# Kernel optimization log

Hardware: AMD Instinct MI355X
Metric: run time of the kernel (lower is better)

## Reference

```python
import jax, jax.numpy as jnp
import numpy as np

N_PATCH = 676
K_SEL = int(676 * 0.8)  # 540
HEADS = 16
LN_EPS = 1e-5


def _layernorm(t, w, b):
    mu = t.mean(-1, keepdims=True)
    var = ((t - mu) ** 2).mean(-1, keepdims=True)
    return (t - mu) * jax.lax.rsqrt(var + LN_EPS) * w + b


def _attention(t, w_qkv, b_qkv, w_out, b_out):
    # t: [S, B, C] (seq-first, like torch nn.MultiheadAttention)
    S, B, C = t.shape
    D = C // HEADS
    qkv = t @ w_qkv.T + b_qkv                       # [S, B, 3C]
    q, k, v = jnp.split(qkv, 3, axis=-1)
    def heads(a):
        return a.reshape(S, B, HEADS, D).transpose(1, 2, 0, 3)  # [B,H,S,D]
    q, k, v = heads(q), heads(k), heads(v)
    scores = jnp.einsum('bhqd,bhkd->bhqk', q, k) / jnp.sqrt(jnp.asarray(D, t.dtype))
    attn = jax.nn.softmax(scores, axis=-1)
    o = jnp.einsum('bhqk,bhkd->bhqd', attn, v)      # [B,H,S,D]
    o = o.transpose(2, 0, 1, 3).reshape(S, B, C)
    return o @ w_out.T + b_out


def _mlp(t, w_fc1, b_fc1, w_fc2, b_fc2):
    h = t @ w_fc1.T + b_fc1
    h = h * jax.nn.sigmoid(1.702 * h)  # CLIP QuickGELU
    return h @ w_fc2.T + b_fc2


def setup_inputs() -> dict:
    key = jax.random.key(0)
    ks = jax.random.split(key, 6)
    C, B, L = 1024, 32, 77
    inp = {
        'x': jax.random.normal(ks[0], (1 + N_PATCH, B, C), jnp.float32),
        'lang_tokens': jax.random.normal(ks[1], (L, B, C), jnp.float32),
        'ln1_w': jnp.ones((C,), jnp.float32),
        'ln1_b': jnp.zeros((C,), jnp.float32),
        'ln2_w': jnp.ones((C,), jnp.float32),
        'ln2_b': jnp.zeros((C,), jnp.float32),
        'w_qkv': jax.random.normal(ks[2], (3 * C, C), jnp.float32) * 0.02,
        'b_qkv': jnp.zeros((3 * C,), jnp.float32),
        'w_out': jax.random.normal(ks[3], (C, C), jnp.float32) * 0.02,
        'b_out': jnp.zeros((C,), jnp.float32),
        'w_fc1': jax.random.normal(ks[4], (4 * C, C), jnp.float32) * 0.02,
        'b_fc1': jnp.zeros((4 * C,), jnp.float32),
        'w_fc2': jax.random.normal(ks[5], (C, 4 * C), jnp.float32) * 0.02,
        'b_fc2': jnp.zeros((C,), jnp.float32),
    }
    return inp


def reference(x, lang_tokens, ln1_w, ln1_b, ln2_w, ln2_b, w_qkv, b_qkv,
              w_out, b_out, w_fc1, b_fc1, w_fc2, b_fc2):
    Nfull, B, C = x.shape
    cls_x = x[:1]            # [1, B, C]
    xt = x[1:]               # [676, B, C]

    # per-token language-alignment score: [676, B]
    score = jnp.einsum('nbc,lbc->nbl', xt, lang_tokens).mean(-1)

    # top-k selection per batch column; torch boolean-mask gather preserves
    # the ORIGINAL token order within the high/low sets -> sort the indices.
    order = jnp.argsort(-score, axis=0)                 # descending
    high_idx = jnp.sort(order[:K_SEL], axis=0)          # [540, B]
    low_idx = jnp.sort(order[K_SEL:], axis=0)           # [136, B]

    delta_x = jnp.take_along_axis(xt, high_idx[:, :, None], axis=0)  # [540,B,C]
    low_x = jnp.take_along_axis(xt, low_idx[:, :, None], axis=0)     # [136,B,C]
    low_score = jnp.take_along_axis(score, low_idx, axis=0)[:, :, None]
    low_tok = (low_x * jax.nn.softmax(low_score, axis=0)).sum(0, keepdims=True)

    seq = jnp.concatenate([cls_x, delta_x, low_tok], axis=0)  # [542, B, C]
    d = _attention(_layernorm(seq, ln1_w, ln1_b), w_qkv, b_qkv, w_out, b_out)

    barange = jnp.arange(B)[None, :]
    temple = jnp.zeros_like(xt)
    temple = temple.at[high_idx, barange].set(d[1:-1])
    temple = temple.at[low_idx, barange].set(
        jnp.broadcast_to(d[-1:], (N_PATCH - K_SEL, B, C)))

    xt = xt + temple
    cls_x = cls_x + d[:1]
    x = jnp.concatenate([cls_x, xt], axis=0)
    x = x + _mlp(_layernorm(x, ln2_w, ln2_b), w_fc1, b_fc1, w_fc2, b_fc2)
    return x
```

## Files before the change

kernel.cpp:

```cpp
#include <hip/hip_runtime.h>
#include <hip/hip_bf16.h>

typedef unsigned short u16;
typedef __attribute__((ext_vector_type(4))) float f32x4;
typedef __attribute__((ext_vector_type(8))) short s16x8;

#define DEVI __device__ __forceinline__

static constexpr int NPATCH = 676;
static constexpr int KSEL   = 540;
static constexpr int NLOW   = 136;
static constexpr int BB     = 32;
static constexpr int CC     = 1024;
static constexpr int S      = 542;
static constexpr int SP     = 576;
static constexpr int M1P    = SP * BB;
static constexpr int NTOK   = 677;
static constexpr int M2     = NTOK * BB;
static constexpr int M2P    = 21760;
static constexpr int NKT    = SP / 64;
static constexpr int NQC    = 5;

DEVI u16 f2bf(float f) {
  unsigned u = __float_as_uint(f);
  u += 0x7fffu + ((u >> 16) & 1u);
  return (u16)(u >> 16);
}
DEVI float bf2f(u16 h) { return __uint_as_float(((unsigned)h) << 16); }
DEVI float ex2(float x) { float r; asm("v_exp_f32 %0, %1" : "=v"(r) : "v"(x)); return r; }

DEVI void gld16(const void* g, void* l) {
  __builtin_amdgcn_global_load_lds((const __attribute__((address_space(1))) void*)g,
                                   (__attribute__((address_space(3))) void*)l,
                                   16, 0, 0);
}

DEVI void BAR() {
  asm volatile("" ::: "memory");
  __builtin_amdgcn_s_barrier();
  asm volatile("" ::: "memory");
}
#define LGKM0() do { asm volatile("s_waitcnt lgkmcnt(0)" ::: "memory"); \
                     __builtin_amdgcn_sched_barrier(0); } while (0)
#define VMC(N) asm volatile("s_waitcnt vmcnt(" #N ")" ::: "memory")


__global__ void k_f2bf4(const float* __restrict__ in, u16* __restrict__ out, int n4) {
  int i = blockIdx.x * blockDim.x + threadIdx.x;
  if (i >= n4) return;
  float4 v = ((const float4*)in)[i];
  unsigned long long p = (unsigned long long)f2bf(v.x)
                       | ((unsigned long long)f2bf(v.y) << 16)
                       | ((unsigned long long)f2bf(v.z) << 32)
                       | ((unsigned long long)f2bf(v.w) << 48);
  *(unsigned long long*)&out[(long)i * 4] = p;
}

__global__ void k_langmean(const float* __restrict__ lang, float* __restrict__ lm) {
  int b = blockIdx.x, t = threadIdx.x;
  float a0 = 0, a1 = 0, a2 = 0, a3 = 0;
  for (int l = 0; l < 77; l++) {
    float4 v = ((const float4*)(lang + ((long)l * BB + b) * CC))[t];
    a0 += v.x; a1 += v.y; a2 += v.z; a3 += v.w;
  }
  const float inv = 1.f / 77.f;
  float4 o; o.x = a0 * inv; o.y = a1 * inv; o.z = a2 * inv; o.w = a3 * inv;
  ((float4*)(lm + b * CC))[t] = o;
}

__global__ void k_score(const float* __restrict__ x, const float* __restrict__ lm,
                        float* __restrict__ score) {
  int nb = blockIdx.x;
  int n = nb >> 5, b = nb & 31;
  int t = threadIdx.x;
  float4 xv = ((const float4*)(x + ((long)(n + 1) * BB + b) * CC))[t];
  float4 lv = ((const float4*)(lm + b * CC))[t];
  float s = xv.x * lv.x + xv.y * lv.y + xv.z * lv.z + xv.w * lv.w;
  for (int m = 1; m < 64; m <<= 1) s += __shfl_xor(s, m);
  __shared__ float sm[4];
  if ((t & 63) == 0) sm[t >> 6] = s;
  __syncthreads();
  if (t == 0) score[n * BB + b] = sm[0] + sm[1] + sm[2] + sm[3];
}

__global__ void k_select(const float* __restrict__ score, float* __restrict__ wall,
                         int* __restrict__ rowmap, int* __restrict__ selsrc,
                         int* __restrict__ lowlist) {
  int b = blockIdx.x, t = threadIdx.x;
  __shared__ float sc[NPATCH];
  __shared__ int hf[NPATCH];
  __shared__ float red[2];
  if (t < NPATCH) sc[t] = score[t * BB + b];
  __syncthreads();
  int high = 0;
  if (t < NPATCH) {
    float s = sc[t];
    int r = 0;
    for (int m = 0; m < NPATCH; m++) {
      float sm_ = sc[m];
      r += (sm_ > s) || (sm_ == s && m < t);
    }
    high = (r < KSEL);
    hf[t] = high;
  }
  __syncthreads();
  if (t < NPATCH) {
    int p = 0;
    for (int m = 0; m < t; m++) p += hf[m];
    if (high) {
      rowmap[b * NPATCH + t] = 1 + p;
      selsrc[b * S + 1 + p] = t + 1;
    } else {
      rowmap[b * NPATCH + t] = S - 1;
      lowlist[b * NLOW + (t - p)] = t;
    }
  }
  if (t == 0) selsrc[b * S + 0] = 0;
  __syncthreads();
  if (t == 0) {
    float m = -3e38f;
    for (int i = 0; i < NPATCH; i++) if (!hf[i]) m = fmaxf(m, sc[i]);
    float d = 0;
    for (int i = 0; i < NPATCH; i++) if (!hf[i]) d += __expf(sc[i] - m);
    red[0] = m; red[1] = d;
  }
  __syncthreads();
  if (t < NPATCH) wall[b * NPATCH + t] = hf[t] ? 0.f : __expf(sc[t] - red[0]) / red[1];
}

__global__ void k_lowtok(const float* __restrict__ x, const float* __restrict__ wall,
                         const int* __restrict__ lowlist, float* __restrict__ lowtok) {
  int b = blockIdx.x, ch = blockIdx.y;
  int c = ch * 256 + threadIdx.x;
  float acc = 0.f;
  for (int i = 0; i < NLOW; i++) {
    int n = lowlist[b * NLOW + i];
    acc += wall[b * NPATCH + n] * x[((long)(n + 1) * BB + b) * CC + c];
  }
  lowtok[b * CC + c] = acc;
}

__global__ void k_lnseq(const float* __restrict__ x, const float* __restrict__ lowtok,
                        const int* __restrict__ selsrc, const float* __restrict__ w,
                        const float* __restrict__ bias, u16* __restrict__ out) {
  int s = blockIdx.x, b = blockIdx.y, t = threadIdx.x;
  u16* orow = out + ((long)b * SP + s) * CC;
  if (s >= S) { *(unsigned long long*)&orow[4 * t] = 0ULL; return; }
  const float* src;
  if (s == 0)          src = x + (long)b * CC;
  else if (s == S - 1) src = lowtok + (long)b * CC;
  else                 src = x + ((long)selsrc[b * S + s] * BB + b) * CC;
  float4 v = ((const float4*)src)[t];
  float ss = v.x + v.y + v.z + v.w;
  float s2 = v.x * v.x + v.y * v.y + v.z * v.z + v.w * v.w;
  for (int k = 1; k < 64; k <<= 1) { ss += __shfl_xor(ss, k); s2 += __shfl_xor(s2, k); }
  __shared__ float sa[4], sb[4];
  if ((t & 63) == 0) { sa[t >> 6] = ss; sb[t >> 6] = s2; }
  __syncthreads();
  ss = sa[0] + sa[1] + sa[2] + sa[3];
  s2 = sb[0] + sb[1] + sb[2] + sb[3];
  float mu = ss * (1.f / CC);
  float var = s2 * (1.f / CC) - mu * mu;
  float rs = rsqrtf(var + 1e-5f);
  int c = 4 * t;
  unsigned long long p = (unsigned long long)f2bf((v.x - mu) * rs * w[c]     + bias[c])
                       | ((unsigned long long)f2bf((v.y - mu) * rs * w[c + 1] + bias[c + 1]) << 16)
                       | ((unsigned long long)f2bf((v.z - mu) * rs * w[c + 2] + bias[c + 2]) << 32)
                       | ((unsigned long long)f2bf((v.w - mu) * rs * w[c + 3] + bias[c + 3]) << 48);
  *(unsigned long long*)&orow[4 * t] = p;
}

__global__ void k_scatln(const float* __restrict__ x, const u16* __restrict__ dbuf,
                         const int* __restrict__ rowmap, const float* __restrict__ w,
                         const float* __restrict__ bias, float* __restrict__ out,
                         u16* __restrict__ lnout) {
  int m = blockIdx.x, t = threadIdx.x;
  u16* orow = lnout + (long)m * CC;
  if (m >= M2) { *(unsigned long long*)&orow[4 * t] = 0ULL; return; }
  int nf = m >> 5, b = m & 31;
  int srow = (nf == 0) ? 0 : rowmap[b * NPATCH + (nf - 1)];
  float4 xv = ((const float4*)(x + (long)m * CC))[t];
  unsigned long long dp = *(const unsigned long long*)&dbuf[((long)b * SP + srow) * CC + 4 * t];
  float4 v;
  v.x = xv.x + bf2f((u16)(dp));
  v.y = xv.y + bf2f((u16)(dp >> 16));
  v.z = xv.z + bf2f((u16)(dp >> 32));
  v.w = xv.w + bf2f((u16)(dp >> 48));
  ((float4*)(out + (long)m * CC))[t] = v;
  float ss = v.x + v.y + v.z + v.w;
  float s2 = v.x * v.x + v.y * v.y + v.z * v.z + v.w * v.w;
  for (int k = 1; k < 64; k <<= 1) { ss += __shfl_xor(ss, k); s2 += __shfl_xor(s2, k); }
  __shared__ float sa[4], sb[4];
  if ((t & 63) == 0) { sa[t >> 6] = ss; sb[t >> 6] = s2; }
  __syncthreads();
  ss = sa[0] + sa[1] + sa[2] + sa[3];
  s2 = sb[0] + sb[1] + sb[2] + sb[3];
  float mu = ss * (1.f / CC);
  float var = s2 * (1.f / CC) - mu * mu;
  float rs = rsqrtf(var + 1e-5f);
  int c = 4 * t;
  unsigned long long p = (unsigned long long)f2bf((v.x - mu) * rs * w[c]     + bias[c])
                       | ((unsigned long long)f2bf((v.y - mu) * rs * w[c + 1] + bias[c + 1]) << 16)
                       | ((unsigned long long)f2bf((v.z - mu) * rs * w[c + 2] + bias[c + 2]) << 32)
                       | ((unsigned long long)f2bf((v.w - mu) * rs * w[c + 3] + bias[c + 3]) << 48);
  *(unsigned long long*)&orow[4 * t] = p;
}


struct Epi {
  const float* bias;
  u16* obf;
  float* of;
  u16 *qb, *kb, *vtb;
  int mvalid, ldc;
};

DEVI void stage_half(u16* dst, const u16* src, int ld) {
  int t = threadIdx.x;
  int c = t & 7;
  int r0 = t >> 3;
  gld16(src + (long)r0 * ld + ((c ^ (r0 & 7)) << 3), dst + (t << 3));
  int r1 = r0 + 64;
  gld16(src + (long)r1 * ld + ((c ^ (r1 & 7)) << 3), dst + 4096 + (t << 3));
}

DEVI s16x8 frag(const u16* half, int rh, int kk, int h4) {
  int chunk = ((kk << 2) | h4) ^ (rh & 7);
  return *(const s16x8*)(half + rh * 64 + chunk * 8);
}

template<int MODE>
__global__ __launch_bounds__(512, 2) void k_gemm8(const u16* __restrict__ A, int lda,
                                                  const u16* __restrict__ Bw, int ldb,
                                                  int K, Epi e) {
  __shared__ __align__(16) u16 lds[2][2][2][8192];
  int t = threadIdx.x;
  int lane = t & 63, w = t >> 6;
  int h4 = lane >> 4, r = lane & 15;
  int wr = w >> 2, wc = w & 3;
  int MBk = gridDim.x, NBk = gridDim.y;
  int nwg = MBk * NBk;
  int orig = blockIdx.y * MBk + blockIdx.x;
  int q8 = nwg >> 3, r8 = nwg & 7, xcd = orig & 7, rk = orig >> 3;
  int wgid = (xcd < r8 ? xcd * (q8 + 1) : r8 * (q8 + 1) + (xcd - r8) * q8) + rk;
  int bm = wgid / NBk, bn = wgid % NBk;

  const u16* Asrc = A + (long)bm * 256 * lda;
  const u16* Bsrc = Bw + (long)bn * 256 * ldb;
  int NT = K >> 6;

  f32x4 acc[8][4];
#pragma unroll
  for (int i = 0; i < 8; i++)
#pragma unroll
    for (int j = 0; j < 4; j++) acc[i][j] = {0.f, 0.f, 0.f, 0.f};

  stage_half(lds[0][0][0], Asrc, lda);
  stage_half(lds[0][0][1], Asrc + (long)128 * lda, lda);
  stage_half(lds[0][1][0], Bsrc, ldb);
  stage_half(lds[0][1][1], Bsrc + (long)128 * ldb, ldb);
  {
    const u16* B1 = Bsrc + (NT > 1 ? 64 : 0);
    stage_half(lds[1][1][0], B1, ldb);
    stage_half(lds[1][1][1], B1 + (long)128 * ldb, ldb);
  }
  VMC(4);
  BAR();

  for (int kt = 0; kt < NT; kt++) {
    int buf = kt & 1;
    const u16* Ah = lds[buf][0][wr];
    const u16* Bh = lds[buf][1][wc >> 1];
    int rbB = (wc & 1) << 6;
    int ka = (kt + 1 < NT) ? kt + 1 : NT - 1;
    int kb = (kt + 2 < NT) ? kt + 2 : NT - 1;
    const u16* Aps = Asrc + ka * 64;
    const u16* Bps = Bsrc + kb * 64;
    u16* AdL = lds[(kt + 1) & 1][0][0];
    u16* AdH = lds[(kt + 1) & 1][0][1];
    u16* BdL = lds[buf][1][0];
    u16* BdH = lds[buf][1][1];

    s16x8 a8[8], b8[8];
#pragma unroll
    for (int i = 0; i < 4; i++) {
      a8[i * 2]     = frag(Ah, i * 16 + r, 0, h4);
      a8[i * 2 + 1] = frag(Ah, i * 16 + r, 1, h4);
    }
#pragma unroll
    for (int j = 0; j < 2; j++) {
      b8[j * 2]     = frag(Bh, rbB + j * 16 + r, 0, h4);
      b8[j * 2 + 1] = frag(Bh, rbB + j * 16 + r, 1, h4);
    }
    stage_half(AdL, Aps, lda);
    BAR(); LGKM0();
    __builtin_amdgcn_s_setprio(1);
#pragma unroll
    for (int i = 0; i < 4; i++)
#pragma unroll
      for (int j = 0; j < 2; j++) {
        acc[i][j] = __builtin_amdgcn_mfma_f32_16x16x32_bf16(a8[i * 2],     b8[j * 2],     acc[i][j], 0, 0, 0);
        acc[i][j] = __builtin_amdgcn_mfma_f32_16x16x32_bf16(a8[i * 2 + 1], b8[j * 2 + 1], acc[i][j], 0, 0, 0);
      }
    __builtin_amdgcn_s_setprio(0);
    BAR();
#pragma unroll
    for (int j = 0; j < 2; j++) {
      b8[4 + j * 2]     = frag(Bh, rbB + (j + 2) * 16 + r, 0, h4);
      b8[4 + j * 2 + 1] = frag(Bh, rbB + (j + 2) * 16 + r, 1, h4);
    }
    stage_half(AdH, Aps + (long)128 * lda, lda);
    BAR(); LGKM0();
    __builtin_amdgcn_s_setprio(1);
#pragma unroll
    for (int i = 0; i < 4; i++)
#pragma unroll
      for (int j = 0; j < 2; j++) {
        acc[i][j + 2] = __builtin_amdgcn_mfma_f32_16x16x32_bf16(a8[i * 2],     b8[4 + j * 2],     acc[i][j + 2], 0, 0, 0);
        acc[i][j + 2] = __builtin_amdgcn_mfma_f32_16x16x32_bf16(a8[i * 2 + 1], b8[4 + j * 2 + 1], acc[i][j + 2], 0, 0, 0);
      }
    __builtin_amdgcn_s_setprio(0);
    BAR();
#pragma unroll
    for (int i = 0; i < 4; i++) {
      a8[i * 2]     = frag(Ah, (i + 4) * 16 + r, 0, h4);
      a8[i * 2 + 1] = frag(Ah, (i + 4) * 16 + r, 1, h4);
    }
    stage_half(BdL, Bps, ldb);
    BAR(); LGKM0();
    __builtin_amdgcn_s_setprio(1);
#pragma unroll
    for (int i = 0; i < 4; i++)
#pragma unroll
      for (int j = 0; j < 2; j++) {
        acc[i + 4][j] = __builtin_amdgcn_mfma_f32_16x16x32_bf16(a8[i * 2],     b8[j * 2],     acc[i + 4][j], 0, 0, 0);
        acc[i + 4][j] = __builtin_amdgcn_mfma_f32_16x16x32_bf16(a8[i * 2 + 1], b8[j * 2 + 1], acc[i + 4][j], 0, 0, 0);
      }
    __builtin_amdgcn_s_setprio(0);
    BAR();
    stage_half(BdH, Bps + (long)128 * ldb, ldb);
    BAR();
    __builtin_amdgcn_s_setprio(1);
#pragma unroll
    for (int i = 0; i < 4; i++)
#pragma unroll
      for (int j = 0; j < 2; j++) {
        acc[i + 4][j + 2] = __builtin_amdgcn_mfma_f32_16x16x32_bf16(a8[i * 2],     b8[4 + j * 2],     acc[i + 4][j + 2], 0, 0, 0);
        acc[i + 4][j + 2] = __builtin_amdgcn_mfma_f32_16x16x32_bf16(a8[i * 2 + 1], b8[4 + j * 2 + 1], acc[i + 4][j + 2], 0, 0, 0);
      }
    __builtin_amdgcn_s_setprio(0);
    VMC(4);
    BAR();
  }

  const float QSC = 0.125f * 1.44269504088896f;
#pragma unroll
  for (int i = 0; i < 8; i++) {
    int m0 = bm * 256 + wr * 128 + i * 16 + 4 * h4;
#pragma unroll
    for (int j = 0; j < 4; j++) {
      int n = bn * 256 + wc * 64 + j * 16 + r;
      float bias = (MODE == 3 && e.bias == nullptr) ? 0.f : e.bias[n];
      if (MODE == 0) {
        int part = n >> 10, cc = n & 1023;
        int hh = cc >> 6, dd = cc & 63;
        int b0 = m0 / SP, s0 = m0 % SP;
        if (part == 2) {
          u16 pk[4];
#pragma unroll
          for (int tt = 0; tt < 4; tt++) pk[tt] = f2bf(acc[i][j][tt] + bias);
          *(unsigned long long*)&e.vtb[((long)(b0 * 16 + hh) * 64 + dd) * SP + s0] =
              *(unsigned long long*)pk;
        } else {
          u16* dst = (part == 0 ? e.qb : e.kb) + ((long)(b0 * 16 + hh) * SP + s0) * 64 + dd;
          float scl = (part == 0) ? QSC : 1.f;
#pragma unroll
          for (int tt = 0; tt < 4; tt++) dst[tt * 64] = f2bf((acc[i][j][tt] + bias) * scl);
        }
      } else if (MODE == 1) {
#pragma unroll
        for (int tt = 0; tt < 4; tt++)
          e.obf[(long)(m0 + tt) * e.ldc + n] = f2bf(acc[i][j][tt] + bias);
      } else if (MODE == 2) {
#pragma unroll
        for (int tt = 0; tt < 4; tt++) {
          float v = acc[i][j][tt] + bias;
          v = v / (1.f + __expf(-1.702f * v));
          e.obf[(long)(m0 + tt) * e.ldc + n] = f2bf(v);
        }
      } else {
#pragma unroll
        for (int tt = 0; tt < 4; tt++) {
          int m = m0 + tt;
          if (m < e.mvalid) e.of[(long)m * CC + n] += acc[i][j][tt] + bias;
        }
      }
    }
  }
}


DEVI void stage64(u16* dst, const u16* src, int ld) {
  int t = threadIdx.x;
  int c = t & 7, r0 = t >> 3;
  gld16(src + (long)r0 * ld + ((c ^ (r0 & 7)) << 3), dst + t * 8);
  int r1 = r0 + 32;
  gld16(src + (long)r1 * ld + ((c ^ (r1 & 7)) << 3), dst + 2048 + t * 8);
}

__global__ __launch_bounds__(256, 4) void k_attn2(const u16* __restrict__ qb,
                                                  const u16* __restrict__ kb,
                                                  const u16* __restrict__ vtb,
                                                  u16* __restrict__ aout) {
  __shared__ __align__(16) u16 Kt[2][4096];
  __shared__ __align__(16) u16 Vt[2][4096];
  __shared__ __align__(16) u16 Pl[4][1024];

  int nwg = gridDim.x;
  int orig = blockIdx.x;
  int q8 = nwg >> 3, r8 = nwg & 7, xcd = orig & 7, rk = orig >> 3;
  int wgid = (xcd < r8 ? xcd * (q8 + 1) : r8 * (q8 + 1) + (xcd - r8) * q8) + rk;
  int bh = wgid / NQC, qc = wgid % NQC;
  int b = bh >> 4, hh = bh & 15;
  int t = threadIdx.x, w = t >> 6, lane = t & 63;
  int h4 = lane >> 4, r = lane & 15;

  const u16* Q  = qb  + (long)bh * SP * 64;
  const u16* Kg = kb  + (long)bh * SP * 64;
  const u16* Vg = vtb + (long)bh * 64 * SP;

  int qt[2];
  bool act[2];
  s16x8 aq0[2], aq1[2];
  f32x4 o[2][4];
  float mM[2][4], lL[2][4];
#pragma unroll
  for (int sub = 0; sub < 2; sub++) {
    qt[sub] = qc * 8 + w * 2 + sub;
    act[sub] = qt[sub] < SP / 16;
    if (act[sub]) {
      aq0[sub] = *(const s16x8*)&Q[(qt[sub] * 16 + r) * 64 + h4 * 8];
      aq1[sub] = *(const s16x8*)&Q[(qt[sub] * 16 + r) * 64 + 32 + h4 * 8];
    }
#pragma unroll
    for (int i = 0; i < 4; i++) { o[sub][i] = {0.f, 0.f, 0.f, 0.f}; mM[sub][i] = -1e30f; lL[sub][i] = 0.f; }
  }

  stage64(Kt[0], Kg, 64);
  stage64(Vt[0], Vg, SP);
  VMC(0);
  BAR();

  for (int kt = 0; kt < NKT; kt++) {
    int cur = kt & 1;
    if (kt + 1 < NKT) {
      stage64(Kt[cur ^ 1], Kg + (kt + 1) * 64 * 64, 64);
      stage64(Vt[cur ^ 1], Vg + (kt + 1) * 64, SP);
    }
    int kv0 = kt * 64;
    const u16* Kc = Kt[cur];
    const u16* Vc = Vt[cur];
#pragma unroll
    for (int sub = 0; sub < 2; sub++) {
      if (!act[sub]) continue;
      f32x4 sf[4];
#pragma unroll
      for (int f = 0; f < 4; f++) {
        sf[f] = {0.f, 0.f, 0.f, 0.f};
        sf[f] = __builtin_amdgcn_mfma_f32_16x16x32_bf16(aq0[sub], frag(Kc, f * 16 + r, 0, h4), sf[f], 0, 0, 0);
        sf[f] = __builtin_amdgcn_mfma_f32_16x16x32_bf16(aq1[sub], frag(Kc, f * 16 + r, 1, h4), sf[f], 0, 0, 0);
      }
      if (kv0 + 64 > S) {
#pragma unroll
        for (int f = 0; f < 4; f++)
          if (kv0 + f * 16 + r >= S) {
#pragma unroll
            for (int tt = 0; tt < 4; tt++) sf[f][tt] = -1e30f;
          }
      }
      float mx[4];
#pragma unroll
      for (int tt = 0; tt < 4; tt++)
        mx[tt] = fmaxf(fmaxf(sf[0][tt], sf[1][tt]), fmaxf(sf[2][tt], sf[3][tt]));
      for (int msk = 1; msk < 16; msk <<= 1) {
#pragma unroll
        for (int tt = 0; tt < 4; tt++) mx[tt] = fmaxf(mx[tt], __shfl_xor(mx[tt], msk));
      }
      int need = 0;
#pragma unroll
      for (int tt = 0; tt < 4; tt++) need |= (mx[tt] > mM[sub][tt] + 8.f);
      if (__any(need)) {
#pragma unroll
        for (int tt = 0; tt < 4; tt++) {
          float mn = fmaxf(mM[sub][tt], mx[tt]);
          float sc = ex2(mM[sub][tt] - mn);
          mM[sub][tt] = mn;
          lL[sub][tt] *= sc;
#pragma unroll
          for (int nf = 0; nf < 4; nf++) o[sub][nf][tt] *= sc;
        }
      }
      float rs[4];
#pragma unroll
      for (int tt = 0; tt < 4; tt++) {
        float m_ = mM[sub][tt];
        float p0 = ex2(sf[0][tt] - m_), p1 = ex2(sf[1][tt] - m_);
        float p2 = ex2(sf[2][tt] - m_), p3 = ex2(sf[3][tt] - m_);
        sf[0][tt] = p0; sf[1][tt] = p1; sf[2][tt] = p2; sf[3][tt] = p3;
        rs[tt] = (p0 + p1) + (p2 + p3);
      }
      for (int msk = 1; msk < 16; msk <<= 1) {
#pragma unroll
        for (int tt = 0; tt < 4; tt++) rs[tt] += __shfl_xor(rs[tt], msk);
      }
#pragma unroll
      for (int tt = 0; tt < 4; tt++) lL[sub][tt] += rs[tt];
      u16* Pw = Pl[w];
#pragma unroll
      for (int f = 0; f < 4; f++)
#pragma unroll
        for (int tt = 0; tt < 4; tt++) {
          int q = 4 * h4 + tt;
          int chunk = (f * 2 + (r >> 3)) ^ (q & 7);
          Pw[q * 64 + chunk * 8 + (r & 7)] = f2bf(sf[f][tt]);
        }
      s16x8 pa0 = frag(Pw, r, 0, h4);
      s16x8 pa1 = frag(Pw, r, 1, h4);
#pragma unroll
      for (int nf = 0; nf < 4; nf++) {
        o[sub][nf] = __builtin_amdgcn_mfma_f32_16x16x32_bf16(pa0, frag(Vc, nf * 16 + r, 0, h4), o[sub][nf], 0, 0, 0);
        o[sub][nf] = __builtin_amdgcn_mfma_f32_16x16x32_bf16(pa1, frag(Vc, nf * 16 + r, 1, h4), o[sub][nf], 0, 0, 0);
      }
    }
    VMC(0);
    BAR();
  }

#pragma unroll
  for (int sub = 0; sub < 2; sub++) {
    if (!act[sub]) continue;
    float inv[4];
#pragma unroll
    for (int tt = 0; tt < 4; tt++) inv[tt] = 1.f / lL[sub][tt];
#pragma unroll
    for (int nf = 0; nf < 4; nf++)
#pragma unroll
      for (int tt = 0; tt < 4; tt++) {
        int q = qt[sub] * 16 + 4 * h4 + tt;
        if (q < S) aout[((long)b * SP + q) * CC + hh * 64 + nf * 16 + r] = f2bf(o[sub][nf][tt] * inv[tt]);
      }
  }
}


extern "C" void kernel_launch(void* const* d_in, const int* in_sizes, int n_in,
                              void* d_out, int out_size, void* d_ws, size_t ws_size,
                              hipStream_t stream) {
  const float* x    = (const float*)d_in[0];
  const float* lang = (const float*)d_in[1];
  const float* ln1w = (const float*)d_in[2];
  const float* ln1b = (const float*)d_in[3];
  const float* ln2w = (const float*)d_in[4];
  const float* ln2b = (const float*)d_in[5];
  const float* wqkv = (const float*)d_in[6];
  const float* bqkv = (const float*)d_in[7];
  const float* wout = (const float*)d_in[8];
  const float* bout = (const float*)d_in[9];
  const float* wfc1 = (const float*)d_in[10];
  const float* bfc1 = (const float*)d_in[11];
  const float* wfc2 = (const float*)d_in[12];
  const float* bfc2 = (const float*)d_in[13];
  float* out = (float*)d_out;
  char* ws = (char*)d_ws;
  const size_t MiB = 1ull << 20;

  float* lm      = (float*)(ws + 0 * MiB);
  float* score   = (float*)(ws + 1 * MiB);
  float* wall    = (float*)(ws + 2 * MiB);
  int*   rowmap  = (int*)  (ws + 3 * MiB);
  int*   selsrc  = (int*)  (ws + 4 * MiB);
  int*   lowlist = (int*)  (ws + 5 * MiB);
  float* lowtok  = (float*)(ws + 6 * MiB);
  u16* wqb  = (u16*)(ws + 7 * MiB);
  u16* wob  = (u16*)(ws + 13 * MiB);
  u16* wf1b = (u16*)(ws + 15 * MiB);
  u16* wf2b = (u16*)(ws + 23 * MiB);
  u16* qbuf = (u16*)(ws + 31 * MiB);
  u16* kbuf = (u16*)(ws + 67 * MiB);
  u16* vtb  = (u16*)(ws + 103 * MiB);
  u16* regA = (u16*)(ws + 139 * MiB);
  u16* lnseq = regA;
  u16* aout  = regA;
  u16* dbuf  = vtb;
  u16* ln2bf = qbuf;
  u16* hbuf  = (u16*)(ws + 74 * MiB);

  {
    int n4;
    n4 = 3072 * 1024 / 4; k_f2bf4<<<(n4 + 255) / 256, 256, 0, stream>>>(wqkv, wqb, n4);
    n4 = 1024 * 1024 / 4; k_f2bf4<<<(n4 + 255) / 256, 256, 0, stream>>>(wout, wob, n4);
    n4 = 4096 * 1024 / 4; k_f2bf4<<<(n4 + 255) / 256, 256, 0, stream>>>(wfc1, wf1b, n4);
    n4 = 1024 * 4096 / 4; k_f2bf4<<<(n4 + 255) / 256, 256, 0, stream>>>(wfc2, wf2b, n4);
  }

  k_langmean<<<BB, 256, 0, stream>>>(lang, lm);
  k_score<<<NPATCH * BB, 256, 0, stream>>>(x, lm, score);
  k_select<<<BB, 1024, 0, stream>>>(score, wall, rowmap, selsrc, lowlist);
  k_lowtok<<<dim3(BB, 4), 256, 0, stream>>>(x, wall, lowlist, lowtok);
  k_lnseq<<<dim3(SP, BB), 256, 0, stream>>>(x, lowtok, selsrc, ln1w, ln1b, lnseq);

  {
    Epi e = {};
    e.bias = bqkv; e.qb = qbuf; e.kb = kbuf; e.vtb = vtb; e.mvalid = M1P;
    k_gemm8<0><<<dim3(M1P / 256, 3072 / 256), 512, 0, stream>>>(lnseq, 1024, wqb, 1024, 1024, e);
  }

  k_attn2<<<BB * 16 * NQC, 256, 0, stream>>>(qbuf, kbuf, vtb, aout);

  {
    Epi e = {};
    e.bias = bout; e.obf = dbuf; e.mvalid = M1P; e.ldc = 1024;
    k_gemm8<1><<<dim3(M1P / 256, 1024 / 256), 512, 0, stream>>>(aout, 1024, wob, 1024, 1024, e);
  }

  k_scatln<<<M2P, 256, 0, stream>>>(x, dbuf, rowmap, ln2w, ln2b, out, ln2bf);

  for (int c = 0; c < 2; c++) {
    Epi e2 = {};
    e2.bias = bfc1 + c * 2048; e2.obf = hbuf; e2.mvalid = M2P; e2.ldc = 2048;
    k_gemm8<2><<<dim3(M2P / 256, 2048 / 256), 512, 0, stream>>>(ln2bf, 1024, wf1b + (long)c * 2048 * 1024, 1024, 1024, e2);
    Epi e3 = {};
    e3.bias = (c == 0 ? bfc2 : nullptr); e3.of = out; e3.mvalid = M2;
    k_gemm8<3><<<dim3(M2P / 256, 1024 / 256), 512, 0, stream>>>(hbuf, 2048, wf2b + c * 2048, 4096, 2048, e3);
  }
}
```

Before: 1.177 ms.

## Replace 256x256 pipelined GEMM with simpler 128x128 double-buffered kernel

Swaps the hand-scheduled 256x256 tile, 8-wave GEMM, with its interleaved staging, priority hints and fine-grained barriers, for a 128x128 tile, 4-wave kernel. The new kernel uses K-steps of 32 with plain double buffering and a new swizzled LDS layout. All four projection/MLP GEMMs launch with four times as many blocks and higher occupancy. The cost is lower data reuse per tile, more global and LDS traffic per FLOP, and dropping the carefully overlapped schedule.

```diff
diff --git a/kernel.cpp b/kernel.cpp
--- a/kernel.cpp
+++ b/kernel.cpp
@@ -40,8 +40,6 @@
   __builtin_amdgcn_s_barrier();
   asm volatile("" ::: "memory");
 }
-#define LGKM0() do { asm volatile("s_waitcnt lgkmcnt(0)" ::: "memory"); \
-                     __builtin_amdgcn_sched_barrier(0); } while (0)
 #define VMC(N) asm volatile("s_waitcnt vmcnt(" #N ")" ::: "memory")
 
 
@@ -215,13 +213,30 @@
   int mvalid, ldc;
 };
 
-DEVI void stage_half(u16* dst, const u16* src, int ld) {
+DEVI void stage32(u16* dst, const u16* src, int ld) {
   int t = threadIdx.x;
-  int c = t & 7;
-  int r0 = t >> 3;
-  gld16(src + (long)r0 * ld + ((c ^ (r0 & 7)) << 3), dst + (t << 3));
-  int r1 = r0 + 64;
-  gld16(src + (long)r1 * ld + ((c ^ (r1 & 7)) << 3), dst + 4096 + (t << 3));
+#pragma unroll
+  for (int q = 0; q < 2; q++) {
+    int s = t + q * 256;
+    int R = s >> 3, clp = s & 7;
+    int lc = clp ^ (R & 7);
+    int m = 2 * R + (lc >> 2), kc = lc & 3;
+    gld16(src + (long)m * ld + kc * 8, dst + s * 8);
+  }
+}
+
+DEVI s16x8 frag32(const u16* tile, int m, int h4) {
+  int R = m >> 1;
+  int phys = ((((m & 1) << 2) | h4) ^ (R & 7));
+  return *(const s16x8*)(tile + R * 64 + phys * 8);
+}
+
+DEVI void stage64(u16* dst, const u16* src, int ld) {
+  int t = threadIdx.x;
+  int c = t & 7, r0 = t >> 3;
+  gld16(src + (long)r0 * ld + ((c ^ (r0 & 7)) << 3), dst + t * 8);
+  int r1 = r0 + 32;
+  gld16(src + (long)r1 * ld + ((c ^ (r1 & 7)) << 3), dst + 2048 + t * 8);
 }
 
 DEVI s16x8 frag(const u16* half, int rh, int kk, int h4) {
@@ -230,14 +245,14 @@
 }
 
 template<int MODE>
-__global__ __launch_bounds__(512, 2) void k_gemm8(const u16* __restrict__ A, int lda,
+__global__ __launch_bounds__(256, 4) void k_gemm3(const u16* __restrict__ A, int lda,
                                                   const u16* __restrict__ Bw, int ldb,
                                                   int K, Epi e) {
-  __shared__ __align__(16) u16 lds[2][2][2][8192];
+  __shared__ __align__(16) u16 lds[2][2][4096];
   int t = threadIdx.x;
   int lane = t & 63, w = t >> 6;
   int h4 = lane >> 4, r = lane & 15;
-  int wr = w >> 2, wc = w & 3;
+  int wr = w >> 1, wc = w & 1;
   int MBk = gridDim.x, NBk = gridDim.y;
   int nwg = MBk * NBk;
   int orig = blockIdx.y * MBk + blockIdx.x;
@@ -245,121 +260,48 @@
   int wgid = (xcd < r8 ? xcd * (q8 + 1) : r8 * (q8 + 1) + (xcd - r8) * q8) + rk;
   int bm = wgid / NBk, bn = wgid % NBk;
 
-  const u16* Asrc = A + (long)bm * 256 * lda;
-  const u16* Bsrc = Bw + (long)bn * 256 * ldb;
-  int NT = K >> 6;
-
-  f32x4 acc[8][4];
-#pragma unroll
-  for (int i = 0; i < 8; i++)
+  const u16* Asrc = A + (long)bm * 128 * lda;
+  const u16* Bsrc = Bw + (long)bn * 128 * ldb;
+  int NT = K >> 5;
+
+  f32x4 acc[4][4];
+#pragma unroll
+  for (int i = 0; i < 4; i++)
 #pragma unroll
     for (int j = 0; j < 4; j++) acc[i][j] = {0.f, 0.f, 0.f, 0.f};
 
-  stage_half(lds[0][0][0], Asrc, lda);
-  stage_half(lds[0][0][1], Asrc + (long)128 * lda, lda);
-  stage_half(lds[0][1][0], Bsrc, ldb);
-  stage_half(lds[0][1][1], Bsrc + (long)128 * ldb, ldb);
-  {
-    const u16* B1 = Bsrc + (NT > 1 ? 64 : 0);
-    stage_half(lds[1][1][0], B1, ldb);
-    stage_half(lds[1][1][1], B1 + (long)128 * ldb, ldb);
-  }
-  VMC(4);
-  BAR();
+  stage32(lds[0][0], Asrc, lda);
+  stage32(lds[0][1], Bsrc, ldb);
+  __syncthreads();
 
   for (int kt = 0; kt < NT; kt++) {
-    int buf = kt & 1;
-    const u16* Ah = lds[buf][0][wr];
-    const u16* Bh = lds[buf][1][wc >> 1];
-    int rbB = (wc & 1) << 6;
-    int ka = (kt + 1 < NT) ? kt + 1 : NT - 1;
-    int kb = (kt + 2 < NT) ? kt + 2 : NT - 1;
-    const u16* Aps = Asrc + ka * 64;
-    const u16* Bps = Bsrc + kb * 64;
-    u16* AdL = lds[(kt + 1) & 1][0][0];
-    u16* AdH = lds[(kt + 1) & 1][0][1];
-    u16* BdL = lds[buf][1][0];
-    u16* BdH = lds[buf][1][1];
-
-    s16x8 a8[8], b8[8];
-#pragma unroll
-    for (int i = 0; i < 4; i++) {
-      a8[i * 2]     = frag(Ah, i * 16 + r, 0, h4);
-      a8[i * 2 + 1] = frag(Ah, i * 16 + r, 1, h4);
-    }
-#pragma unroll
-    for (int j = 0; j < 2; j++) {
-      b8[j * 2]     = frag(Bh, rbB + j * 16 + r, 0, h4);
-      b8[j * 2 + 1] = frag(Bh, rbB + j * 16 + r, 1, h4);
-    }
-    stage_half(AdL, Aps, lda);
-    BAR(); LGKM0();
-    __builtin_amdgcn_s_setprio(1);
+    int cur = kt & 1;
+    if (kt + 1 < NT) {
+      stage32(lds[cur ^ 1][0], Asrc + (kt + 1) * 32, lda);
+      stage32(lds[cur ^ 1][1], Bsrc + (kt + 1) * 32, ldb);
+    }
+    const u16* At = lds[cur][0];
+    const u16* Bt = lds[cur][1];
+    s16x8 af[4], bf[4];
+#pragma unroll
+    for (int i = 0; i < 4; i++) af[i] = frag32(At, wr * 64 + i * 16 + r, h4);
+#pragma unroll
+    for (int j = 0; j < 4; j++) bf[j] = frag32(Bt, wc * 64 + j * 16 + r, h4);
 #pragma unroll
     for (int i = 0; i < 4; i++)
 #pragma unroll
-      for (int j = 0; j < 2; j++) {
-        acc[i][j] = __builtin_amdgcn_mfma_f32_16x16x32_bf16(a8[i * 2],     b8[j * 2],     acc[i][j], 0, 0, 0);
-        acc[i][j] = __builtin_amdgcn_mfma_f32_16x16x32_bf16(a8[i * 2 + 1], b8[j * 2 + 1], acc[i][j], 0, 0, 0);
-      }
-    __builtin_amdgcn_s_setprio(0);
-    BAR();
-#pragma unroll
-    for (int j = 0; j < 2; j++) {
-      b8[4 + j * 2]     = frag(Bh, rbB + (j + 2) * 16 + r, 0, h4);
-      b8[4 + j * 2 + 1] = frag(Bh, rbB + (j + 2) * 16 + r, 1, h4);
-    }
-    stage_half(AdH, Aps + (long)128 * lda, lda);
-    BAR(); LGKM0();
-    __builtin_amdgcn_s_setprio(1);
-#pragma unroll
-    for (int i = 0; i < 4; i++)
-#pragma unroll
-      for (int j = 0; j < 2; j++) {
-        acc[i][j + 2] = __builtin_amdgcn_mfma_f32_16x16x32_bf16(a8[i * 2],     b8[4 + j * 2],     acc[i][j + 2], 0, 0, 0);
-        acc[i][j + 2] = __builtin_amdgcn_mfma_f32_16x16x32_bf16(a8[i * 2 + 1], b8[4 + j * 2 + 1], acc[i][j + 2], 0, 0, 0);
-      }
-    __builtin_amdgcn_s_setprio(0);
-    BAR();
-#pragma unroll
-    for (int i = 0; i < 4; i++) {
-      a8[i * 2]     = frag(Ah, (i + 4) * 16 + r, 0, h4);
-      a8[i * 2 + 1] = frag(Ah, (i + 4) * 16 + r, 1, h4);
-    }
-    stage_half(BdL, Bps, ldb);
-    BAR(); LGKM0();
-    __builtin_amdgcn_s_setprio(1);
-#pragma unroll
-    for (int i = 0; i < 4; i++)
-#pragma unroll
-      for (int j = 0; j < 2; j++) {
-        acc[i + 4][j] = __builtin_amdgcn_mfma_f32_16x16x32_bf16(a8[i * 2],     b8[j * 2],     acc[i + 4][j], 0, 0, 0);
-        acc[i + 4][j] = __builtin_amdgcn_mfma_f32_16x16x32_bf16(a8[i * 2 + 1], b8[j * 2 + 1], acc[i + 4][j], 0, 0, 0);
-      }
-    __builtin_amdgcn_s_setprio(0);
-    BAR();
-    stage_half(BdH, Bps + (long)128 * ldb, ldb);
-    BAR();
-    __builtin_amdgcn_s_setprio(1);
-#pragma unroll
-    for (int i = 0; i < 4; i++)
-#pragma unroll
-      for (int j = 0; j < 2; j++) {
-        acc[i + 4][j + 2] = __builtin_amdgcn_mfma_f32_16x16x32_bf16(a8[i * 2],     b8[4 + j * 2],     acc[i + 4][j + 2], 0, 0, 0);
-        acc[i + 4][j + 2] = __builtin_amdgcn_mfma_f32_16x16x32_bf16(a8[i * 2 + 1], b8[4 + j * 2 + 1], acc[i + 4][j + 2], 0, 0, 0);
-      }
-    __builtin_amdgcn_s_setprio(0);
-    VMC(4);
-    BAR();
+      for (int j = 0; j < 4; j++)
+        acc[i][j] = __builtin_amdgcn_mfma_f32_16x16x32_bf16(af[i], bf[j], acc[i][j], 0, 0, 0);
+    __syncthreads();
   }
 
   const float QSC = 0.125f * 1.44269504088896f;
 #pragma unroll
-  for (int i = 0; i < 8; i++) {
-    int m0 = bm * 256 + wr * 128 + i * 16 + 4 * h4;
+  for (int i = 0; i < 4; i++) {
+    int m0 = bm * 128 + wr * 64 + i * 16 + 4 * h4;
 #pragma unroll
     for (int j = 0; j < 4; j++) {
-      int n = bn * 256 + wc * 64 + j * 16 + r;
+      int n = bn * 128 + wc * 64 + j * 16 + r;
       float bias = (MODE == 3 && e.bias == nullptr) ? 0.f : e.bias[n];
       if (MODE == 0) {
         int part = n >> 10, cc = n & 1023;
@@ -399,14 +341,6 @@
   }
 }
 
-
-DEVI void stage64(u16* dst, const u16* src, int ld) {
-  int t = threadIdx.x;
-  int c = t & 7, r0 = t >> 3;
-  gld16(src + (long)r0 * ld + ((c ^ (r0 & 7)) << 3), dst + t * 8);
-  int r1 = r0 + 32;
-  gld16(src + (long)r1 * ld + ((c ^ (r1 & 7)) << 3), dst + 2048 + t * 8);
-}
 
 __global__ __launch_bounds__(256, 4) void k_attn2(const u16* __restrict__ qb,
                                                   const u16* __restrict__ kb,
@@ -612,7 +546,7 @@
   {
     Epi e = {};
     e.bias = bqkv; e.qb = qbuf; e.kb = kbuf; e.vtb = vtb; e.mvalid = M1P;
-    k_gemm8<0><<<dim3(M1P / 256, 3072 / 256), 512, 0, stream>>>(lnseq, 1024, wqb, 1024, 1024, e);
+    k_gemm3<0><<<dim3(M1P / 128, 3072 / 128), 256, 0, stream>>>(lnseq, 1024, wqb, 1024, 1024, e);
   }
 
   k_attn2<<<BB * 16 * NQC, 256, 0, stream>>>(qbuf, kbuf, vtb, aout);
@@ -620,7 +554,7 @@
   {
     Epi e = {};
     e.bias = bout; e.obf = dbuf; e.mvalid = M1P; e.ldc = 1024;
-    k_gemm8<1><<<dim3(M1P / 256, 1024 / 256), 512, 0, stream>>>(aout, 1024, wob, 1024, 1024, e);
+    k_gemm3<1><<<dim3(M1P / 128, 1024 / 128), 256, 0, stream>>>(aout, 1024, wob, 1024, 1024, e);
   }
 
   k_scatln<<<M2P, 256, 0, stream>>>(x, dbuf, rowmap, ln2w, ln2b, out, ln2bf);
@@ -628,9 +562,9 @@
   for (int c = 0; c < 2; c++) {
     Epi e2 = {};
     e2.bias = bfc1 + c * 2048; e2.obf = hbuf; e2.mvalid = M2P; e2.ldc = 2048;
-    k_gemm8<2><<<dim3(M2P / 256, 2048 / 256), 512, 0, stream>>>(ln2bf, 1024, wf1b + (long)c * 2048 * 1024, 1024, 1024, e2);
+    k_gemm3<2><<<dim3(M2P / 128, 2048 / 128), 256, 0, stream>>>(ln2bf, 1024, wf1b + (long)c * 2048 * 1024, 1024, 1024, e2);
     Epi e3 = {};
     e3.bias = (c == 0 ? bfc2 : nullptr); e3.of = out; e3.mvalid = M2;
-    k_gemm8<3><<<dim3(M2P / 256, 1024 / 256), 512, 0, stream>>>(hbuf, 2048, wf2b + c * 2048, 4096, 2048, e3);
-  }
-}
+    k_gemm3<3><<<dim3(M2P / 128, 1024 / 128), 256, 0, stream>>>(hbuf, 2048, wf2b + c * 2048, 4096, 2048, e3);
+  }
+}
```

Measured after the change: 1.100 ms. 6.6% less time.
